# Performance work log

Measured on AMD Instinct MI355X. Metric: run time of the kernel, lower is better.

## Reference

```python
import jax, jax.numpy as jnp
import numpy as np

T, B, E, H = 2048, 2, 1024, 16
DH = E // H
SCALE = DH ** -0.5
NEG = jnp.finfo(jnp.float32).min


def setup_inputs() -> dict:
    key = jax.random.key(0)
    ks = jax.random.split(key, 10)
    s = 0.02
    query = jax.random.normal(ks[0], (T, B, E), dtype=jnp.float32)
    key_padding_mask = jax.random.randint(ks[1], (B, T), 0, 2).astype(bool)
    # causal additive mask, broadcastable over (bsz, heads, tgt, src)
    causal = jnp.triu(jnp.ones((T, T), dtype=bool), k=1)
    attn_mask = jnp.where(causal, NEG, 0.0).astype(jnp.float32)[None, None]
    Wq = jax.random.normal(ks[2], (E, E), jnp.float32) * s
    bq = jax.random.normal(ks[3], (E,), jnp.float32) * s
    Wk = jax.random.normal(ks[4], (E, E), jnp.float32) * s
    bk = jax.random.normal(ks[5], (E,), jnp.float32) * s
    Wv = jax.random.normal(ks[6], (E, E), jnp.float32) * s
    bv = jax.random.normal(ks[7], (E,), jnp.float32) * s
    Wo = jax.random.normal(ks[8], (E, E), jnp.float32) * s
    bo = jax.random.normal(ks[9], (E,), jnp.float32) * s
    return {"query": query, "key_padding_mask": key_padding_mask, "attn_mask": attn_mask,
            "Wq": Wq, "bq": bq, "Wk": Wk, "bk": bk, "Wv": Wv, "bv": bv, "Wo": Wo, "bo": bo}


def _heads(x):
    # [T, B, E] -> [B, H, T, DH]
    return x.reshape(T, B, H, DH).transpose(1, 2, 0, 3)


def reference(query, key_padding_mask, attn_mask, Wq, bq, Wk, bk, Wv, bv, Wo, bo):
    # projections (torch Linear: x @ W.T + b); q scaled as in module
    q = _heads((query @ Wq.T + bq) * SCALE)          # [B,H,T,DH]
    k = _heads(query @ Wk.T + bk)                    # [B,H,S,DH] (self-attn: S=T)
    v = _heads(query @ Wv.T + bv)
    scores = jnp.einsum('bhtd,bhsd->bhts', q, k)     # [B,H,T,S]
    scores = scores + attn_mask                      # additive causal mask
    # key_padding_mask True -> masked_fill with dtype min
    scores = jnp.where(key_padding_mask[:, None, None, :], NEG, scores)
    probs = jax.nn.softmax(scores, axis=-1)
    ctx = jnp.einsum('bhts,bhsd->bhtd', probs, v)    # [B,H,T,DH]
    ctx = ctx.transpose(2, 0, 1, 3).reshape(T, B, E) # back to [T,B,E]
    return ctx @ Wo.T + bo
```

## Files before the change

### kernel.cpp

```cpp
#include <hip/hip_runtime.h>
#include <hip/hip_bf16.h>
#include <stdint.h>

typedef unsigned short u16;
typedef uint32_t u32;
typedef unsigned long long u64;
typedef __attribute__((ext_vector_type(8))) short bf16x8;
typedef __attribute__((ext_vector_type(4))) float f32x4;
typedef __attribute__((ext_vector_type(16))) float f32x16;
typedef __attribute__((ext_vector_type(4))) u32 u32x4;

#define T_SEQ 2048

__device__ __forceinline__ float bf2f(u16 u) {
  union { u32 i; float f; } v; v.i = ((u32)u) << 16; return v.f;
}
__device__ __forceinline__ u16 f2bf(float f) {
  union { float f; u32 i; } v; v.f = f;
  u32 u = v.i;
  return (u16)((u + 0x7fffu + ((u >> 16) & 1u)) >> 16);
}
__device__ __forceinline__ u32 pack2bf(float lo, float hi) {
  return (u32)f2bf(lo) | ((u32)f2bf(hi) << 16);
}

__device__ __forceinline__ void gload_lds16(const void* g, void* l) {
  __builtin_amdgcn_global_load_lds(
      (const __attribute__((address_space(1))) void*)g,
      (__attribute__((address_space(3))) void*)l, 16, 0, 0);
}

__global__ __launch_bounds__(256) void cvt_kernel(const float* __restrict__ src,
                                                  u16* __restrict__ dst, int n) {
  int i = (blockIdx.x * 256 + threadIdx.x) * 4;
  if (i + 3 < n) {
    const float4 v = *(const float4*)(src + i);
    ushort4 o;
    o.x = f2bf(v.x); o.y = f2bf(v.y); o.z = f2bf(v.z); o.w = f2bf(v.w);
    *(ushort4*)(dst + i) = o;
  }
}

__global__ __launch_bounds__(256) void cvt4_kernel(
    const float* __restrict__ s0, const float* __restrict__ s1,
    const float* __restrict__ s2, const float* __restrict__ s3,
    u16* __restrict__ dst) {
  const int z = blockIdx.y;
  const float* src = (z == 0) ? s0 : (z == 1) ? s1 : (z == 2) ? s2 : s3;
  int i = (blockIdx.x * 256 + threadIdx.x) * 4;
  const float4 v = *(const float4*)(src + i);
  ushort4 o;
  o.x = f2bf(v.x); o.y = f2bf(v.y); o.z = f2bf(v.z); o.w = f2bf(v.w);
  *(ushort4*)(dst + (size_t)z * 1048576 + i) = o;
}

__device__ __forceinline__ void gemm_core_128x64(
    f32x4 acc[2][4], const u16* __restrict__ A, const u16* __restrict__ Bw,
    int bm, int bn, u16* As, u16* Bs)
{
  const int tid = threadIdx.x;
  const int w = tid >> 6, lane = tid & 63, g = lane >> 4, c = lane & 15;
  for (int k0 = 0; k0 < 1024; k0 += 64) {
    __syncthreads();
    #pragma unroll
    for (int is = 0; is < 4; ++is) {
      int o = (is*4 + w)*1024 + lane*16;
      int row = o >> 7, c16 = (o >> 4) & 7;
      gload_lds16(A + (size_t)(bm*128 + row)*1024 + k0 + (c16 ^ (row & 7))*8,
                  (char*)As + (is*4 + w)*1024);
    }
    #pragma unroll
    for (int is = 0; is < 2; ++is) {
      int o = (is*4 + w)*1024 + lane*16;
      int row = o >> 7, c16 = (o >> 4) & 7;
      gload_lds16(Bw + (size_t)(bn*64 + row)*1024 + k0 + (c16 ^ (row & 7))*8,
                  (char*)Bs + (is*4 + w)*1024);
    }
    __syncthreads();
    bf16x8 af[2][2], bfr[4][2];
    #pragma unroll
    for (int mf = 0; mf < 2; ++mf)
      #pragma unroll
      for (int kc = 0; kc < 2; ++kc) {
        int row = w*32 + mf*16 + c;
        int colb = kc*64 + g*16;
        af[mf][kc] = *(const bf16x8*)((const char*)As + row*128 + (colb ^ ((row & 7) << 4)));
      }
    #pragma unroll
    for (int nf = 0; nf < 4; ++nf)
      #pragma unroll
      for (int kc = 0; kc < 2; ++kc) {
        int row = nf*16 + c;
        int colb = kc*64 + g*16;
        bfr[nf][kc] = *(const bf16x8*)((const char*)Bs + row*128 + (colb ^ ((row & 7) << 4)));
      }
    #pragma unroll
    for (int mf = 0; mf < 2; ++mf)
      #pragma unroll
      for (int nf = 0; nf < 4; ++nf)
        #pragma unroll
        for (int kc = 0; kc < 2; ++kc)
          acc[mf][nf] = __builtin_amdgcn_mfma_f32_16x16x32_bf16(
              af[mf][kc], bfr[nf][kc], acc[mf][nf], 0, 0, 0);
  }
}

__global__ __launch_bounds__(256, 2) void gemm_qkv(
    const u16* __restrict__ Abf, const u16* __restrict__ Wbf,
    const float* __restrict__ bq, const float* __restrict__ bk,
    const float* __restrict__ bv, u16* __restrict__ qkvh)
{
  __shared__ __align__(16) u16 As[128*64];
  __shared__ __align__(16) u16 Bs[64*64];
  f32x4 acc[2][4];
  #pragma unroll
  for (int mf = 0; mf < 2; ++mf)
    #pragma unroll
    for (int nf = 0; nf < 4; ++nf) acc[mf][nf] = (f32x4){0.f,0.f,0.f,0.f};
  const int z = blockIdx.z;
  gemm_core_128x64(acc, Abf, Wbf + (size_t)z*1048576, blockIdx.x, blockIdx.y, As, Bs);
  const float* bias = (z == 0) ? bq : (z == 1) ? bk : bv;
  const float scl = (z == 0) ? 0.125f : 1.0f;
  u16* dst = qkvh + (size_t)z * 4194304;
  const int tid = threadIdx.x, w = tid >> 6, lane = tid & 63, g = lane >> 4, c = lane & 15;
  #pragma unroll
  for (int mf = 0; mf < 2; ++mf)
    #pragma unroll
    for (int nf = 0; nf < 4; ++nf) {
      int col = blockIdx.y*64 + nf*16 + c;
      float bcol = bias[col];
      int h = col >> 6, d = col & 63;
      #pragma unroll
      for (int r = 0; r < 4; ++r) {
        int row = blockIdx.x*128 + w*32 + mf*16 + g*4 + r;
        int t = row >> 1, bb = row & 1;
        float v = (acc[mf][nf][r] + bcol) * scl;
        dst[(size_t)(bb*16 + h)*131072 + (size_t)t*64 + d] = f2bf(v);
      }
    }
}

__global__ __launch_bounds__(256, 2) void gemm_out(
    const u16* __restrict__ ctx2, const u16* __restrict__ Wobf,
    const float* __restrict__ bo, float* __restrict__ out)
{
  __shared__ __align__(16) u16 As[128*64];
  __shared__ __align__(16) u16 Bs[64*64];
  f32x4 acc[2][4];
  #pragma unroll
  for (int mf = 0; mf < 2; ++mf)
    #pragma unroll
    for (int nf = 0; nf < 4; ++nf) acc[mf][nf] = (f32x4){0.f,0.f,0.f,0.f};
  gemm_core_128x64(acc, ctx2, Wobf, blockIdx.x, blockIdx.y, As, Bs);
  const int tid = threadIdx.x, w = tid >> 6, lane = tid & 63, g = lane >> 4, c = lane & 15;
  #pragma unroll
  for (int mf = 0; mf < 2; ++mf)
    #pragma unroll
    for (int nf = 0; nf < 4; ++nf) {
      int col = blockIdx.y*64 + nf*16 + c;
      float bcol = bo[col];
      #pragma unroll
      for (int r = 0; r < 4; ++r) {
        int row = blockIdx.x*128 + w*32 + mf*16 + g*4 + r;
        out[(size_t)row*1024 + col] = acc[mf][nf][r] + bcol;
      }
    }
}

__global__ __launch_bounds__(256) void vtrans_kernel(const u16* __restrict__ Vh,
                                                     u16* __restrict__ Vt,
                                                     float* __restrict__ vs) {
  __shared__ u16 tile[64][72];
  const int bh = blockIdx.x >> 5, tc = blockIdx.x & 31;
  const int t0 = tc * 64;
  const int tid = threadIdx.x;
  {
    const int tl = tid >> 2, d0 = (tid & 3) * 16;
    const u16* src = Vh + (size_t)bh*131072 + (size_t)(t0 + tl)*64 + d0;
    bf16x8 a = *(const bf16x8*)src;
    bf16x8 b2 = *(const bf16x8*)(src + 8);
    #pragma unroll
    for (int j = 0; j < 8; ++j) {
      tile[d0 + j][tl] = (u16)a[j];
      tile[d0 + 8 + j][tl] = (u16)b2[j];
    }
  }
  __syncthreads();
  {
    const int d = tid >> 2, tq = (tid & 3) * 16;
    bf16x8 o0, o1;
    float s = 0.f;
    #pragma unroll
    for (int j = 0; j < 8; ++j) {
      u16 x0 = tile[d][tq + j], x1 = tile[d][tq + 8 + j];
      o0[j] = (short)x0; o1[j] = (short)x1;
      s += bf2f(x0) + bf2f(x1);
    }
    u16* dst = Vt + (size_t)bh*131072 + (size_t)d*2048 + t0 + tq;
    *(bf16x8*)dst = o0;
    *(bf16x8*)(dst + 8) = o1;
    s += __shfl_xor(s, 1, 64);
    s += __shfl_xor(s, 2, 64);
    if ((tid & 3) == 0) atomicAdd(&vs[bh*64 + d], s);
  }
}

#define ZERO16 (f32x16){0.f,0.f,0.f,0.f,0.f,0.f,0.f,0.f,0.f,0.f,0.f,0.f,0.f,0.f,0.f,0.f}
#define NEGINF (-__builtin_inff())

__global__ __launch_bounds__(64, 2) void flash_attn(
    const u16* __restrict__ Qh, const u16* __restrict__ Kh,
    const u16* __restrict__ Vt, const int* __restrict__ kpm,
    const float* __restrict__ vsum, u16* __restrict__ ctx2)
{
  const int lane = threadIdx.x;
  const int l31 = lane & 31, hi = lane >> 5;

  const int id = blockIdx.x;
  const int xcd = id & 7, rest = id >> 3;
  const int bh = xcd * 4 + (rest & 3);
  const int pr = rest >> 2;
  const int p = pr & 7, kk = pr >> 3;
  const int qp = p*4 + (kk >> 1);
  const int qt = (kk & 1) ? (63 - qp) : qp;
  const int b = bh >> 4, h = bh & 15;
  const int q0 = qt * 32;
  const size_t hbase = (size_t)bh * 131072;
  const int nt = (q0 >> 6) + 1;
  const int q = q0 + l31;

  bf16x8 qfrag[4];
  #pragma unroll
  for (int kt = 0; kt < 4; ++kt)
    qfrag[kt] = *(const bf16x8*)(Qh + hbase + (size_t)q*64 + kt*16 + hi*8);

  bf16x8 kreg[2][4];
  #pragma unroll
  for (int sub = 0; sub < 2; ++sub)
    #pragma unroll
    for (int kt = 0; kt < 4; ++kt)
      kreg[sub][kt] = *(const bf16x8*)(Kh + hbase + (size_t)(sub*32 + l31)*64 + kt*16 + hi*8);

  int kpmv_cur = kpm[b*T_SEQ + lane];
  int kpmv_nxt = 0;

  float mrow = NEGINF, lrow = 0.f;
  f32x16 cacc0 = ZERO16, cacc1 = ZERO16;

  for (int t = 0; t < nt; ++t) {
    const int s0 = t * 64;
    const bool notLast = (t + 1 < nt);

    bf16x8 vf[2][4];
    #pragma unroll
    for (int db = 0; db < 2; ++db)
      #pragma unroll
      for (int ks = 0; ks < 4; ++ks)
        vf[db][ks] = *(const bf16x8*)(Vt + hbase + (size_t)(db*32 + l31)*2048 + s0 + ks*16 + hi*8);

    f32x16 st0 = ZERO16, st1 = ZERO16;
    __builtin_amdgcn_s_setprio(1);
    #pragma unroll
    for (int kt = 0; kt < 4; ++kt) {
      st0 = __builtin_amdgcn_mfma_f32_32x32x16_bf16(kreg[0][kt], qfrag[kt], st0, 0, 0, 0);
      st1 = __builtin_amdgcn_mfma_f32_32x32x16_bf16(kreg[1][kt], qfrag[kt], st1, 0, 0, 0);
    }
    __builtin_amdgcn_s_setprio(0);

    if (notLast) {
      #pragma unroll
      for (int sub = 0; sub < 2; ++sub)
        #pragma unroll
        for (int kt = 0; kt < 4; ++kt)
          kreg[sub][kt] = *(const bf16x8*)(Kh + hbase + (size_t)(s0 + 64 + sub*32 + l31)*64 + kt*16 + hi*8);
      kpmv_nxt = kpm[b*T_SEQ + s0 + 64 + lane];
    }

    {
      const u64 mask = __ballot(kpmv_cur != 0);
      const u32 m0 = (u32)mask, m1 = (u32)(mask >> 32);
      const u64 m4 = mask >> 4;
      const u32 m4l = (u32)m4, m4h = (u32)(m4 >> 32);
      const u32 w0 = hi ? m4l : m0;
      const u32 w1 = hi ? m4h : m1;
      const int lim = q - s0 - 4*hi;
      #pragma unroll
      for (int m = 0; m < 4; ++m) {
        u32 nib0 = (w0 >> (m*8)) & 15u;
        u32 nib1 = (w1 >> (m*8)) & 15u;
        if (!notLast) {
          int t0c = lim - m*8;       int c0 = min(max(t0c + 1, 0), 4);
          int t1c = lim - 32 - m*8;  int c1 = min(max(t1c + 1, 0), 4);
          nib0 |= (0xFu << c0) & 0xFu;
          nib1 |= (0xFu << c1) & 0xFu;
        }
        #pragma unroll
        for (int r = 0; r < 4; ++r) {
          if ((nib0 >> r) & 1) st0[m*4 + r] = NEGINF;
          if ((nib1 >> r) & 1) st1[m*4 + r] = NEGINF;
        }
      }
      float rm = st0[0];
      #pragma unroll
      for (int i = 1; i < 16; ++i) rm = fmaxf(rm, st0[i]);
      #pragma unroll
      for (int i = 0; i < 16; ++i) rm = fmaxf(rm, st1[i]);
      rm = fmaxf(rm, __shfl_xor(rm, 32, 64));
      const float mn = fmaxf(mrow, rm);
      const bool dead = (mn == NEGINF);
      const float sc = dead ? 1.f : __expf(mrow - mn);
      mrow = mn;
      float ps = 0.f;
      #pragma unroll
      for (int i = 0; i < 16; ++i) {
        float pv = dead ? 0.f : __expf(st0[i] - mn);
        st0[i] = pv; ps += pv;
      }
      #pragma unroll
      for (int i = 0; i < 16; ++i) {
        float pv = dead ? 0.f : __expf(st1[i] - mn);
        st1[i] = pv; ps += pv;
      }
      ps += __shfl_xor(ps, 32, 64);
      lrow = lrow * sc + ps;
      #pragma unroll
      for (int i = 0; i < 16; ++i) { cacc0[i] *= sc; cacc1[i] *= sc; }
    }

    u32 pk[8][2];
    #pragma unroll
    for (int m = 0; m < 4; ++m) {
      pk[m][0]   = pack2bf(st0[m*4+0], st0[m*4+1]);
      pk[m][1]   = pack2bf(st0[m*4+2], st0[m*4+3]);
      pk[4+m][0] = pack2bf(st1[m*4+0], st1[m*4+1]);
      pk[4+m][1] = pack2bf(st1[m*4+2], st1[m*4+3]);
    }
    bf16x8 pf[4];
    #pragma unroll
    for (int ks = 0; ks < 4; ++ks) {
      u32 own0 = pk[2*ks][0],   own1 = pk[2*ks][1];
      u32 oth0 = pk[2*ks+1][0], oth1 = pk[2*ks+1][1];
      u32 r0 = __shfl_xor(hi ? own0 : oth0, 32, 64);
      u32 r1 = __shfl_xor(hi ? own1 : oth1, 32, 64);
      u32 w0 = hi ? r0 : own0;
      u32 w1 = hi ? r1 : own1;
      u32 w2 = hi ? oth0 : r0;
      u32 w3 = hi ? oth1 : r1;
      u32x4 wv = {w0, w1, w2, w3};
      pf[ks] = __builtin_bit_cast(bf16x8, wv);
    }

    __builtin_amdgcn_s_setprio(1);
    #pragma unroll
    for (int ks = 0; ks < 4; ++ks)
      cacc0 = __builtin_amdgcn_mfma_f32_32x32x16_bf16(vf[0][ks], pf[ks], cacc0, 0, 0, 0);
    #pragma unroll
    for (int ks = 0; ks < 4; ++ks)
      cacc1 = __builtin_amdgcn_mfma_f32_32x32x16_bf16(vf[1][ks], pf[ks], cacc1, 0, 0, 0);
    __builtin_amdgcn_s_setprio(0);

    kpmv_cur = kpmv_nxt;
  }

  const bool dead = (lrow == 0.f);
  const float rl = dead ? 0.f : 1.f / lrow;
  #pragma unroll
  for (int subd = 0; subd < 2; ++subd) {
    #pragma unroll
    for (int m = 0; m < 4; ++m) {
      const int d0 = subd*32 + hi*4 + m*8;
      float v0 = (subd ? cacc1[m*4+0] : cacc0[m*4+0]) * rl;
      float v1 = (subd ? cacc1[m*4+1] : cacc0[m*4+1]) * rl;
      float v2 = (subd ? cacc1[m*4+2] : cacc0[m*4+2]) * rl;
      float v3 = (subd ? cacc1[m*4+3] : cacc0[m*4+3]) * rl;
      if (dead) {
        const float* vs = vsum + bh*64 + d0;
        v0 = vs[0] * (1.0f/2048.0f);
        v1 = vs[1] * (1.0f/2048.0f);
        v2 = vs[2] * (1.0f/2048.0f);
        v3 = vs[3] * (1.0f/2048.0f);
      }
      ushort4 o;
      o.x = f2bf(v0); o.y = f2bf(v1); o.z = f2bf(v2); o.w = f2bf(v3);
      *(ushort4*)(ctx2 + (size_t)(q*2 + b)*1024 + h*64 + d0) = o;
    }
  }
}

extern "C" void kernel_launch(void* const* d_in, const int* in_sizes, int n_in,
                              void* d_out, int out_size, void* d_ws, size_t ws_size,
                              hipStream_t stream) {
  const float* query = (const float*)d_in[0];
  const int*   kpm   = (const int*)d_in[1];
  const float* Wq = (const float*)d_in[3];
  const float* bq = (const float*)d_in[4];
  const float* Wk = (const float*)d_in[5];
  const float* bk = (const float*)d_in[6];
  const float* Wv = (const float*)d_in[7];
  const float* bv = (const float*)d_in[8];
  const float* Wo = (const float*)d_in[9];
  const float* bo = (const float*)d_in[10];

  char* ws = (char*)d_ws;
  u16*   qbf  = (u16*)(ws);
  u16*   Vt   = (u16*)(ws);
  u16*   wbf  = (u16*)(ws + 8388608);
  u16*   qkvh = (u16*)(ws + 16777216);
  u16*   ctx2 = (u16*)(ws + 41943040);
  float* vsum = (float*)(ws + 50331648);

  cvt_kernel<<<dim3(4096), 256, 0, stream>>>(query, qbf, 4194304);
  cvt4_kernel<<<dim3(1024, 4), 256, 0, stream>>>(Wq, Wk, Wv, Wo, wbf);

  hipMemsetAsync(vsum, 0, 2048 * sizeof(float), stream);

  gemm_qkv<<<dim3(32, 16, 3), 256, 0, stream>>>(qbf, wbf, bq, bk, bv, qkvh);
  vtrans_kernel<<<dim3(1024), 256, 0, stream>>>(qkvh + 2*4194304, Vt, vsum);
  flash_attn<<<dim3(2048), 64, 0, stream>>>(qkvh, qkvh + 1*4194304,
                                            Vt, kpm, vsum, ctx2);
  gemm_out<<<dim3(32, 16), 256, 0, stream>>>(ctx2, wbf + 3*1048576, bo, (float*)d_out);
}
```

Baseline: 151.1 us.

## Split long causal attention rows across two blocks and merge partials

Query tiles in the upper half of the causal range are split into two key-range chunks, each handled by its own block. The chunks write unnormalized bf16 partial contexts plus running max and sum, and a new combine kernel merges them, rebalancing load and raising block count. The change also folds log2(e) into the Q scale so the softmax can use exp2, packs probabilities to bf16 by truncation through a byte permute instead of round-to-nearest, and raises the occupancy hint. The cost is an extra launch, partial-result traffic through workspace, and extra rounding from bf16 partials and truncated packing.

```diff
diff --git a/kernel.cpp b/kernel.cpp
--- a/kernel.cpp
+++ b/kernel.cpp
@@ -20,8 +20,19 @@
   u32 u = v.i;
   return (u16)((u + 0x7fffu + ((u >> 16) & 1u)) >> 16);
 }
-__device__ __forceinline__ u32 pack2bf(float lo, float hi) {
-  return (u32)f2bf(lo) | ((u32)f2bf(hi) << 16);
+
+#if __has_builtin(__builtin_amdgcn_exp2f)
+#define EXP2F(x) __builtin_amdgcn_exp2f(x)
+#else
+#define EXP2F(x) exp2f(x)
+#endif
+
+__device__ __forceinline__ u32 permpack(float lo, float hi) {
+#if __has_builtin(__builtin_amdgcn_perm)
+  return __builtin_amdgcn_perm(__float_as_uint(hi), __float_as_uint(lo), 0x07060302u);
+#else
+  return (__float_as_uint(hi) & 0xFFFF0000u) | (__float_as_uint(lo) >> 16);
+#endif
 }
 
 __device__ __forceinline__ void gload_lds16(const void* g, void* l) {
@@ -120,7 +131,7 @@
   const int z = blockIdx.z;
   gemm_core_128x64(acc, Abf, Wbf + (size_t)z*1048576, blockIdx.x, blockIdx.y, As, Bs);
   const float* bias = (z == 0) ? bq : (z == 1) ? bk : bv;
-  const float scl = (z == 0) ? 0.125f : 1.0f;
+  const float scl = (z == 0) ? 0.18033688011112043f : 1.0f;
   u16* dst = qkvh + (size_t)z * 4194304;
   const int tid = threadIdx.x, w = tid >> 6, lane = tid & 63, g = lane >> 4, c = lane & 15;
   #pragma unroll
@@ -208,10 +219,11 @@
 #define ZERO16 (f32x16){0.f,0.f,0.f,0.f,0.f,0.f,0.f,0.f,0.f,0.f,0.f,0.f,0.f,0.f,0.f,0.f}
 #define NEGINF (-__builtin_inff())
 
-__global__ __launch_bounds__(64, 2) void flash_attn(
+__global__ __launch_bounds__(64, 4) void flash_attn(
     const u16* __restrict__ Qh, const u16* __restrict__ Kh,
     const u16* __restrict__ Vt, const int* __restrict__ kpm,
-    const float* __restrict__ vsum, u16* __restrict__ ctx2)
+    const float* __restrict__ vsum, u16* __restrict__ ctx2,
+    u16* __restrict__ pctx, float* __restrict__ pml)
 {
   const int lane = threadIdx.x;
   const int l31 = lane & 31, hi = lane >> 5;
@@ -219,14 +231,17 @@
   const int id = blockIdx.x;
   const int xcd = id & 7, rest = id >> 3;
   const int bh = xcd * 4 + (rest & 3);
-  const int pr = rest >> 2;
-  const int p = pr & 7, kk = pr >> 3;
-  const int qp = p*4 + (kk >> 1);
-  const int qt = (kk & 1) ? (63 - qp) : qp;
+  const int pp = rest >> 2;
+  int qt, ch, NS;
+  if (pp < 32) { qt = pp; ch = 0; NS = 1; }
+  else { int uu = pp - 32; qt = 32 + (uu >> 1); ch = uu & 1; NS = 2; }
   const int b = bh >> 4, h = bh & 15;
   const int q0 = qt * 32;
   const size_t hbase = (size_t)bh * 131072;
-  const int nt = (q0 >> 6) + 1;
+  const int nt = (qt >> 1) + 1;
+  int lo, hicap;
+  if (NS == 1) { lo = 0; hicap = nt; }
+  else { int h1 = nt >> 1; lo = ch ? h1 : 0; hicap = ch ? nt : h1; }
   const int q = q0 + l31;
 
   bf16x8 qfrag[4];
@@ -239,17 +254,18 @@
   for (int sub = 0; sub < 2; ++sub)
     #pragma unroll
     for (int kt = 0; kt < 4; ++kt)
-      kreg[sub][kt] = *(const bf16x8*)(Kh + hbase + (size_t)(sub*32 + l31)*64 + kt*16 + hi*8);
-
-  int kpmv_cur = kpm[b*T_SEQ + lane];
+      kreg[sub][kt] = *(const bf16x8*)(Kh + hbase + (size_t)(lo*64 + sub*32 + l31)*64 + kt*16 + hi*8);
+
+  int kpmv_cur = kpm[b*T_SEQ + lo*64 + lane];
   int kpmv_nxt = 0;
 
   float mrow = NEGINF, lrow = 0.f;
   f32x16 cacc0 = ZERO16, cacc1 = ZERO16;
 
-  for (int t = 0; t < nt; ++t) {
+  for (int t = lo; t < hicap; ++t) {
     const int s0 = t * 64;
-    const bool notLast = (t + 1 < nt);
+    const bool notLast = (t + 1 < hicap);
+    const bool diag = (t == nt - 1);
 
     bf16x8 vf[2][4];
     #pragma unroll
@@ -288,7 +304,7 @@
       for (int m = 0; m < 4; ++m) {
         u32 nib0 = (w0 >> (m*8)) & 15u;
         u32 nib1 = (w1 >> (m*8)) & 15u;
-        if (!notLast) {
+        if (diag) {
           int t0c = lim - m*8;       int c0 = min(max(t0c + 1, 0), 4);
           int t1c = lim - 32 - m*8;  int c1 = min(max(t1c + 1, 0), 4);
           nib0 |= (0xFu << c0) & 0xFu;
@@ -300,25 +316,27 @@
           if ((nib1 >> r) & 1) st1[m*4 + r] = NEGINF;
         }
       }
-      float rm = st0[0];
-      #pragma unroll
-      for (int i = 1; i < 16; ++i) rm = fmaxf(rm, st0[i]);
-      #pragma unroll
-      for (int i = 0; i < 16; ++i) rm = fmaxf(rm, st1[i]);
+      float t8[8];
+      #pragma unroll
+      for (int i = 0; i < 8; ++i)
+        t8[i] = fmaxf(fmaxf(st0[i], st0[i+8]), fmaxf(st1[i], st1[i+8]));
+      float t4a = fmaxf(t8[0], t8[4]), t4b = fmaxf(t8[1], t8[5]);
+      float t4c = fmaxf(t8[2], t8[6]), t4d = fmaxf(t8[3], t8[7]);
+      float rm = fmaxf(fmaxf(t4a, t4b), fmaxf(t4c, t4d));
       rm = fmaxf(rm, __shfl_xor(rm, 32, 64));
       const float mn = fmaxf(mrow, rm);
       const bool dead = (mn == NEGINF);
-      const float sc = dead ? 1.f : __expf(mrow - mn);
+      const float sc = dead ? 1.f : EXP2F(mrow - mn);
       mrow = mn;
       float ps = 0.f;
       #pragma unroll
       for (int i = 0; i < 16; ++i) {
-        float pv = dead ? 0.f : __expf(st0[i] - mn);
+        float pv = dead ? 0.f : EXP2F(st0[i] - mn);
         st0[i] = pv; ps += pv;
       }
       #pragma unroll
       for (int i = 0; i < 16; ++i) {
-        float pv = dead ? 0.f : __expf(st1[i] - mn);
+        float pv = dead ? 0.f : EXP2F(st1[i] - mn);
         st1[i] = pv; ps += pv;
       }
       ps += __shfl_xor(ps, 32, 64);
@@ -330,10 +348,10 @@
     u32 pk[8][2];
     #pragma unroll
     for (int m = 0; m < 4; ++m) {
-      pk[m][0]   = pack2bf(st0[m*4+0], st0[m*4+1]);
-      pk[m][1]   = pack2bf(st0[m*4+2], st0[m*4+3]);
-      pk[4+m][0] = pack2bf(st1[m*4+0], st1[m*4+1]);
-      pk[4+m][1] = pack2bf(st1[m*4+2], st1[m*4+3]);
+      pk[m][0]   = permpack(st0[m*4+0], st0[m*4+1]);
+      pk[m][1]   = permpack(st0[m*4+2], st0[m*4+3]);
+      pk[4+m][0] = permpack(st1[m*4+0], st1[m*4+1]);
+      pk[4+m][1] = permpack(st1[m*4+2], st1[m*4+3]);
     }
     bf16x8 pf[4];
     #pragma unroll
@@ -362,28 +380,89 @@
     kpmv_cur = kpmv_nxt;
   }
 
-  const bool dead = (lrow == 0.f);
-  const float rl = dead ? 0.f : 1.f / lrow;
-  #pragma unroll
-  for (int subd = 0; subd < 2; ++subd) {
-    #pragma unroll
-    for (int m = 0; m < 4; ++m) {
-      const int d0 = subd*32 + hi*4 + m*8;
-      float v0 = (subd ? cacc1[m*4+0] : cacc0[m*4+0]) * rl;
-      float v1 = (subd ? cacc1[m*4+1] : cacc0[m*4+1]) * rl;
-      float v2 = (subd ? cacc1[m*4+2] : cacc0[m*4+2]) * rl;
-      float v3 = (subd ? cacc1[m*4+3] : cacc0[m*4+3]) * rl;
-      if (dead) {
-        const float* vs = vsum + bh*64 + d0;
-        v0 = vs[0] * (1.0f/2048.0f);
-        v1 = vs[1] * (1.0f/2048.0f);
-        v2 = vs[2] * (1.0f/2048.0f);
-        v3 = vs[3] * (1.0f/2048.0f);
-      }
-      ushort4 o;
-      o.x = f2bf(v0); o.y = f2bf(v1); o.z = f2bf(v2); o.w = f2bf(v3);
-      *(ushort4*)(ctx2 + (size_t)(q*2 + b)*1024 + h*64 + d0) = o;
-    }
+  if (NS == 1) {
+    const bool dead = (lrow == 0.f);
+    const float rl = dead ? 0.f : 1.f / lrow;
+    #pragma unroll
+    for (int subd = 0; subd < 2; ++subd) {
+      #pragma unroll
+      for (int m = 0; m < 4; ++m) {
+        const int d0 = subd*32 + hi*4 + m*8;
+        float v0 = (subd ? cacc1[m*4+0] : cacc0[m*4+0]) * rl;
+        float v1 = (subd ? cacc1[m*4+1] : cacc0[m*4+1]) * rl;
+        float v2 = (subd ? cacc1[m*4+2] : cacc0[m*4+2]) * rl;
+        float v3 = (subd ? cacc1[m*4+3] : cacc0[m*4+3]) * rl;
+        if (dead) {
+          const float* vs = vsum + bh*64 + d0;
+          v0 = vs[0] * (1.0f/2048.0f);
+          v1 = vs[1] * (1.0f/2048.0f);
+          v2 = vs[2] * (1.0f/2048.0f);
+          v3 = vs[3] * (1.0f/2048.0f);
+        }
+        ushort4 o;
+        o.x = f2bf(v0); o.y = f2bf(v1); o.z = f2bf(v2); o.w = f2bf(v3);
+        *(ushort4*)(ctx2 + (size_t)(q*2 + b)*1024 + h*64 + d0) = o;
+      }
+    }
+  } else {
+    const int slot = ((bh << 5) + (qt - 32))*2 + ch;
+    u16* pc = pctx + (size_t)slot*2048 + (size_t)l31*64;
+    #pragma unroll
+    for (int subd = 0; subd < 2; ++subd) {
+      #pragma unroll
+      for (int m = 0; m < 4; ++m) {
+        const int d0 = subd*32 + hi*4 + m*8;
+        const f32x16& cc = subd ? cacc1 : cacc0;
+        ushort4 o;
+        o.x = f2bf(cc[m*4+0]); o.y = f2bf(cc[m*4+1]);
+        o.z = f2bf(cc[m*4+2]); o.w = f2bf(cc[m*4+3]);
+        *(ushort4*)(pc + d0) = o;
+      }
+    }
+    if (!hi) {
+      float2 ml; ml.x = mrow; ml.y = lrow;
+      *(float2*)(pml + (size_t)slot*64 + l31*2) = ml;
+    }
+  }
+}
+
+__global__ __launch_bounds__(64) void combine_kernel(
+    const u16* __restrict__ pctx, const float* __restrict__ pml,
+    const float* __restrict__ vsum, u16* __restrict__ ctx2)
+{
+  const int qtm = blockIdx.x, bh = blockIdx.y;
+  const int qt = 32 + qtm;
+  const int b = bh >> 4, h = bh & 15;
+  const int lane = threadIdx.x;
+  const int qr = lane >> 1, d0 = (lane & 1) * 32;
+  const int slot0 = ((bh << 5) + qtm)*2;
+  const float* ml0 = pml + (size_t)slot0*64 + qr*2;
+  const float* ml1 = pml + (size_t)(slot0+1)*64 + qr*2;
+  const float m1 = ml0[0], l1 = ml0[1];
+  const float m2 = ml1[0], l2 = ml1[1];
+  const float ms = fmaxf(m1, m2);
+  bool dead = (ms == NEGINF);
+  const float w1 = dead ? 0.f : EXP2F(m1 - ms);
+  const float w2 = dead ? 0.f : EXP2F(m2 - ms);
+  const float lt = w1*l1 + w2*l2;
+  dead = dead || (lt == 0.f);
+  const float rl = dead ? 0.f : 1.f / lt;
+  const u16* c1 = pctx + ((size_t)slot0*32 + qr)*64 + d0;
+  const u16* c2 = pctx + ((size_t)(slot0+1)*32 + qr)*64 + d0;
+  const int qrow = qt*32 + qr;
+  u16* dst = ctx2 + (size_t)(qrow*2 + b)*1024 + h*64 + d0;
+  #pragma unroll
+  for (int g2 = 0; g2 < 4; ++g2) {
+    bf16x8 a = *(const bf16x8*)(c1 + g2*8);
+    bf16x8 bb = *(const bf16x8*)(c2 + g2*8);
+    bf16x8 o;
+    #pragma unroll
+    for (int j = 0; j < 8; ++j) {
+      float v = (w1*bf2f((u16)a[j]) + w2*bf2f((u16)bb[j])) * rl;
+      if (dead) v = vsum[bh*64 + d0 + g2*8 + j] * (1.0f/2048.0f);
+      o[j] = (short)f2bf(v);
+    }
+    *(bf16x8*)(dst + g2*8) = o;
   }
 }
 
@@ -406,8 +485,10 @@
   u16*   Vt   = (u16*)(ws);
   u16*   wbf  = (u16*)(ws + 8388608);
   u16*   qkvh = (u16*)(ws + 16777216);
+  u16*   pctx = (u16*)(ws + 33554432);
   u16*   ctx2 = (u16*)(ws + 41943040);
   float* vsum = (float*)(ws + 50331648);
+  float* pml  = (float*)(ws + 50339840);
 
   cvt_kernel<<<dim3(4096), 256, 0, stream>>>(query, qbf, 4194304);
   cvt4_kernel<<<dim3(1024, 4), 256, 0, stream>>>(Wq, Wk, Wv, Wo, wbf);
@@ -416,7 +497,8 @@
 
   gemm_qkv<<<dim3(32, 16, 3), 256, 0, stream>>>(qbf, wbf, bq, bk, bv, qkvh);
   vtrans_kernel<<<dim3(1024), 256, 0, stream>>>(qkvh + 2*4194304, Vt, vsum);
-  flash_attn<<<dim3(2048), 64, 0, stream>>>(qkvh, qkvh + 1*4194304,
-                                            Vt, kpm, vsum, ctx2);
+  flash_attn<<<dim3(3072), 64, 0, stream>>>(qkvh, qkvh + 1*4194304,
+                                            Vt, kpm, vsum, ctx2, pctx, pml);
+  combine_kernel<<<dim3(32, 32), 64, 0, stream>>>(pctx, pml, vsum, ctx2);
   gemm_out<<<dim3(32, 16), 256, 0, stream>>>(ctx2, wbf + 3*1048576, bo, (float*)d_out);
 }
```

After: 215.6 us. 42.7% more time.
